# Kernel optimization log

Measured on AMD Instinct MI355X. Metric: run time of the kernel, lower is better.

## Reference

```python
import jax, jax.numpy as jnp
import numpy as np

IMG = 224          # image_size
FMAP = (56, 56)    # feature_map_dims (AdaptiveAvgPool2d((56,56)))
K_REWEIGHT = 3     # self.n_reweight
BLUR_RADIUS = 4    # KNNGaussianBlur(4): kernel 9, sigma 4


def _cdist(a, b):
    # Euclidean pairwise distance, [Na, D] x [Nb, D] -> [Na, Nb]
    a2 = jnp.sum(a * a, axis=1, keepdims=True)            # [Na,1]
    b2 = jnp.sum(b * b, axis=1, keepdims=True).T          # [1,Nb]
    d2 = a2 + b2 - 2.0 * (a @ b.T)
    return jnp.sqrt(jnp.maximum(d2, 0.0))


def _gaussian_blur(x):
    # x: [1,1,H,W]; torchvision GaussianBlur(kernel=9, sigma=4), reflect pad
    r, sigma = BLUR_RADIUS, float(BLUR_RADIUS)
    t = jnp.arange(2 * r + 1, dtype=x.dtype) - r
    g = jnp.exp(-(t * t) / (2.0 * sigma * sigma))
    g = g / jnp.sum(g)
    k2d = jnp.outer(g, g)[None, None]                     # [1,1,9,9]
    xp = jnp.pad(x, ((0, 0), (0, 0), (r, r), (r, r)), mode='reflect')
    return jax.lax.conv_general_dilated(
        xp, k2d, window_strides=(1, 1), padding='VALID',
        dimension_numbers=('NCHW', 'OIHW', 'NCHW'))


def setup_inputs() -> dict:
    key = jax.random.key(0)
    k1, k2 = jax.random.split(key)
    patch = jax.random.normal(k1, (FMAP[0] * FMAP[1], 768), dtype=jnp.float32)
    patch_lib = jax.random.normal(k2, (16384, 768), dtype=jnp.float32)
    mean = jnp.zeros((), dtype=jnp.float32)
    std = jnp.ones((), dtype=jnp.float32)
    return {"patch": patch, "patch_lib": patch_lib, "mean": mean, "std": std}


def reference(patch, patch_lib, mean, std):
    # normalization (method_name != 'Point_MAE' branch)
    p = (patch - mean) / std                               # [N, D]

    dist = _cdist(p, patch_lib)                            # [N, Nlib]
    min_val = jnp.min(dist, axis=1)                        # [N]
    min_idx = jnp.argmin(dist, axis=1)                     # [N]
    s_idx = jnp.argmax(min_val)
    s_star = jnp.max(min_val)

    m_test = p[s_idx]                                      # [D]
    m_star = patch_lib[min_idx[s_idx]]                     # [D]

    # distances of m_star to whole bank, k smallest
    w_dist = jnp.sqrt(jnp.maximum(
        jnp.sum((patch_lib - m_star) ** 2, axis=1), 0.0))  # [Nlib]
    _, nn_idx = jax.lax.top_k(-w_dist, K_REWEIGHT)         # smallest k
    m_star_knn = jnp.linalg.norm(
        m_test[None, :] - patch_lib[nn_idx[1:]], axis=1)   # [k-1]

    D_sqrt = jnp.sqrt(jnp.asarray(patch.shape[1], dtype=p.dtype))
    w = 1.0 - jnp.exp(s_star / D_sqrt) / jnp.sum(jnp.exp(m_star_knn / D_sqrt))
    s = w * s_star

    s_map = min_val.reshape(1, 1, *FMAP)
    s_map = jax.image.resize(s_map, (1, 1, IMG, IMG), method='bilinear')
    s_map = _gaussian_blur(s_map)
    return s, s_map
```

## Files before the change

### kernel.cpp

```cpp
#include <hip/hip_runtime.h>
#include <hip/hip_bf16.h>
#include <stdint.h>

#define N_PATCH 3136
#define N_PATCH_PAD 3200
#define N_LIB   16384
#define DIM     768
#define IMGSZ   224
#define FM      56

#define BK 32
#define KT 24
#define MT 25
#define NTILES 128

#define TAILB 64
#define D2_MARGIN 8.0f

typedef __bf16 bf16_t;
typedef __bf16 bf16x8 __attribute__((ext_vector_type(8)));
typedef __bf16 bf16x4_v __attribute__((ext_vector_type(4)));
typedef float  f32x4  __attribute__((ext_vector_type(4)));

#define FLT_MAX_ 3.402823466e+38f

struct Scal {
  unsigned long long approx_max_pack;
  unsigned long long cand_pack[64];
  int cand[64];
  int cand_count;
  int bar[4];
};

__device__ __forceinline__ float wave_reduce_sum(float v) {
#pragma unroll
  for (int s = 32; s > 0; s >>= 1) v += __shfl_xor(v, s, 64);
  return v;
}

__device__ __forceinline__ float wave_reduce_min(float v) {
#pragma unroll
  for (int s = 32; s > 0; s >>= 1) v = fminf(v, __shfl_xor(v, s, 64));
  return v;
}

__device__ __forceinline__ unsigned long long shfl_xor_u64(unsigned long long v, int mask) {
  unsigned lo = (unsigned)v, hi = (unsigned)(v >> 32);
  lo = __shfl_xor(lo, mask, 64);
  hi = __shfl_xor(hi, mask, 64);
  return ((unsigned long long)hi << 32) | lo;
}

__device__ __forceinline__ void async16(const bf16_t* g, bf16_t* l) {
  __builtin_amdgcn_global_load_lds(
      (const __attribute__((address_space(1))) unsigned int*)g,
      (__attribute__((address_space(3))) unsigned int*)l, 16, 0, 0);
}

__device__ __forceinline__ void grid_bar(int* ctr, int nb) {
  __syncthreads();
  if (threadIdx.x == 0) {
    __threadfence();
    atomicAdd(ctr, 1);
    while (atomicAdd(ctr, 0) < nb) __builtin_amdgcn_s_sleep(8);
    __threadfence();
  }
  __syncthreads();
}

__device__ __forceinline__ float bf16u_to_f(unsigned short u) {
  return __uint_as_float(((unsigned)u) << 16);
}

__global__ void prep_kernel(const float* __restrict__ patch, const float* __restrict__ lib,
                            const float* __restrict__ meanp, const float* __restrict__ stdp,
                            bf16_t* __restrict__ pb, bf16_t* __restrict__ lb,
                            float* __restrict__ a2, float* __restrict__ b2, Scal* sc) {
  int t = threadIdx.x;
  int lane = t & 63;
  if (blockIdx.x == 0) {
    if (t < 64) sc->cand_pack[t] = ~0ULL;
    if (t == 64) { sc->approx_max_pack = 0ULL; sc->cand_count = 0; }
    if (t >= 65 && t < 69) sc->bar[t - 65] = 0;
  }
  if (blockIdx.x < N_PATCH / 4) {
    int row = blockIdx.x * 4 + (t >> 6);
    float mu = meanp[0], sd = stdp[0];
    float acc = 0.f;
#pragma unroll
    for (int k = 0; k < 3; k++) {
      float4 v = ((const float4*)(patch + (size_t)row * DIM))[lane + 64 * k];
      v.x = (v.x - mu) / sd; v.y = (v.y - mu) / sd;
      v.z = (v.z - mu) / sd; v.w = (v.w - mu) / sd;
      bf16x4_v o = {(__bf16)v.x, (__bf16)v.y, (__bf16)v.z, (__bf16)v.w};
      *(bf16x4_v*)(pb + (size_t)row * DIM + (lane + 64 * k) * 4) = o;
      acc += v.x*v.x + v.y*v.y + v.z*v.z + v.w*v.w;
    }
    acc = wave_reduce_sum(acc);
    if (lane == 0) a2[row] = acc;
  } else {
    int row = (blockIdx.x - N_PATCH / 4) * 4 + (t >> 6);
    float acc = 0.f;
#pragma unroll
    for (int k = 0; k < 3; k++) {
      float4 v = ((const float4*)(lib + (size_t)row * DIM))[lane + 64 * k];
      bf16x4_v o = {(__bf16)v.x, (__bf16)v.y, (__bf16)v.z, (__bf16)v.w};
      *(bf16x4_v*)(lb + (size_t)row * DIM + (lane + 64 * k) * 4) = o;
      acc += v.x*v.x + v.y*v.y + v.z*v.z + v.w*v.w;
    }
    acc = wave_reduce_sum(acc);
    if (lane == 0) b2[row] = acc;
  }
}

__global__ __launch_bounds__(256, 3)
void gemm_min_kernel(const bf16_t* __restrict__ pb, const bf16_t* __restrict__ lb,
                     const float* __restrict__ a2, const float* __restrict__ b2,
                     float* __restrict__ part) {
  __shared__ __align__(16) bf16_t As[2][128 * BK];
  __shared__ __align__(16) bf16_t Bs[2][128 * BK];
  __shared__ unsigned smin[128];

  const int t = threadIdx.x;
  const int wave = t >> 6;
  const int lane = t & 63;
  const int l15 = lane & 15;
  const int quad = lane >> 4;
  const int wm = (wave >> 1) * 64;
  const int wn = (wave & 1) * 64;

  const int lid = blockIdx.x;
  const int xcd = lid & 7;
  const int slot = lid >> 3;
  const int ntile = xcd + 8 * (slot / MT);
  const int mtile = slot % MT;
  const int m0 = mtile * 128;
  const int n0 = ntile * 128;

  int ra0 = m0 + (t >> 2);       if (ra0 > N_PATCH - 1) ra0 = N_PATCH - 1;
  int ra1 = m0 + 64 + (t >> 2);  if (ra1 > N_PATCH - 1) ra1 = N_PATCH - 1;
  const bf16_t* gA0 = pb + (size_t)ra0 * DIM + (t & 3) * 8;
  const bf16_t* gA1 = pb + (size_t)ra1 * DIM + (t & 3) * 8;
  const bf16_t* gB0 = lb + (size_t)(n0 + (t >> 2)) * DIM + (t & 3) * 8;
  const bf16_t* gB1 = gB0 + (size_t)64 * DIM;

  if (t < 128) smin[t] = 0xffffffffu;

  {
    bf16_t* la = &As[0][0];
    bf16_t* lb_ = &Bs[0][0];
    async16(gA0, la + t * 8);
    async16(gA1, la + 2048 + t * 8);
    async16(gB0, lb_ + t * 8);
    async16(gB1, lb_ + 2048 + t * 8);
  }
  __syncthreads();

  f32x4 acc[4][4];
#pragma unroll
  for (int mi = 0; mi < 4; mi++)
#pragma unroll
    for (int ni = 0; ni < 4; ni++) { f32x4 z = {0.f,0.f,0.f,0.f}; acc[mi][ni] = z; }

  for (int k = 0; k < KT; ++k) {
    const int cur = k & 1;
    if (k + 1 < KT) {
      const int nxt = cur ^ 1;
      const size_t ko = (size_t)(k + 1) * BK;
      bf16_t* la = &As[nxt][0];
      bf16_t* lb_ = &Bs[nxt][0];
      async16(gA0 + ko, la + t * 8);
      async16(gA1 + ko, la + 2048 + t * 8);
      async16(gB0 + ko, lb_ + t * 8);
      async16(gB1 + ko, lb_ + 2048 + t * 8);
    }

    bf16x8 afr[4], bfr[4];
#pragma unroll
    for (int mi = 0; mi < 4; mi++)
      afr[mi] = *(const bf16x8*)(&As[cur][(wm + mi * 16 + l15) * BK + quad * 8]);
#pragma unroll
    for (int ni = 0; ni < 4; ni++)
      bfr[ni] = *(const bf16x8*)(&Bs[cur][(wn + ni * 16 + l15) * BK + quad * 8]);
#pragma unroll
    for (int mi = 0; mi < 4; mi++)
#pragma unroll
      for (int ni = 0; ni < 4; ni++)
        acc[mi][ni] = __builtin_amdgcn_mfma_f32_16x16x32_bf16(afr[mi], bfr[ni],
                                                              acc[mi][ni], 0, 0, 0);
    __syncthreads();
  }

  float b2n[4];
#pragma unroll
  for (int ni = 0; ni < 4; ni++) b2n[ni] = b2[n0 + wn + ni * 16 + l15];

#pragma unroll
  for (int mi = 0; mi < 4; mi++) {
#pragma unroll
    for (int r = 0; r < 4; r++) {
      int rloc = wm + mi * 16 + quad * 4 + r;
      int mrow = m0 + rloc;
      float a2v = a2[mrow < N_PATCH ? mrow : (N_PATCH - 1)];
      float best = a2v + b2n[0] - 2.0f * acc[mi][0][r];
#pragma unroll
      for (int ni = 1; ni < 4; ni++)
        best = fminf(best, a2v + b2n[ni] - 2.0f * acc[mi][ni][r]);
      best = fmaxf(best, 0.0f);
#pragma unroll
      for (int s = 1; s < 16; s <<= 1)
        best = fminf(best, __shfl_xor(best, s, 64));
      if (l15 == 0) atomicMin(&smin[rloc], __float_as_uint(best));
    }
  }
  __syncthreads();
  if (t < 128) part[(size_t)ntile * N_PATCH_PAD + m0 + t] = __uint_as_float(smin[t]);
}

__device__ __forceinline__ void wave_pick(const Scal* sc, int cnt, int lane,
                                          int* srow, float* sstar, int* ms) {
  unsigned long long pk = 0ULL;
  int rowv = 0, msv = 0;
  if (lane < cnt) {
    unsigned long long cp = sc->cand_pack[lane];
    rowv = sc->cand[lane];
    msv = (int)(cp & 0xffffffffu);
    pk = (cp & 0xffffffff00000000ULL) | (unsigned)(0xffffffffu - (unsigned)rowv);
  }
  unsigned long long m = pk;
#pragma unroll
  for (int s = 1; s < 64; s <<= 1) {
    unsigned long long o = shfl_xor_u64(m, s);
    if (o > m) m = o;
  }
  unsigned long long mask = __ballot(pk == m && lane < cnt);
  int wl = (int)(__ffsll((long long)mask) - 1);
  *srow = __shfl(rowv, wl, 64);
  *ms   = __shfl(msv, wl, 64);
  *sstar = sqrtf(__uint_as_float((unsigned)(m >> 32)));
}

__global__ __launch_bounds__(256, 2)
void tail_kernel(const float* __restrict__ part, float* __restrict__ min_val,
                 const float* __restrict__ patch, const float* __restrict__ lib,
                 const bf16_t* __restrict__ lb,
                 const float* __restrict__ meanp, const float* __restrict__ stdp,
                 Scal* __restrict__ sc, float* __restrict__ wdist2,
                 float* __restrict__ out0, float* __restrict__ outmap) {
  __shared__ union {
    unsigned long long sl[768];
    float rs[40 * 40];
  } sm;
  __shared__ float redbuf[4];
  __shared__ int s_cnt;

  const int t = threadIdx.x;
  const int b = blockIdx.x;
  const int wave = t >> 6, lane = t & 63;

  {
    int row = b * 256 + t;
    if (row < N_PATCH) {
      float m = FLT_MAX_;
#pragma unroll 8
      for (int nt = 0; nt < NTILES; nt++)
        m = fminf(m, part[(size_t)nt * N_PATCH_PAD + row]);
      float v = sqrtf(m);
      min_val[row] = v;
      unsigned long long mp = (((unsigned long long)__float_as_uint(v)) << 32) |
                              (unsigned)(0xffffffffu - (unsigned)row);
      atomicMax(&sc->approx_max_pack, mp);
    }
  }
  grid_bar(&sc->bar[0], TAILB);

  if (b == 0) {
    float amax = __uint_as_float((unsigned)(atomicMax(&sc->approx_max_pack, 0ULL) >> 32));
    for (int i = t; i < N_PATCH; i += 256) {
      if (min_val[i] >= amax - 0.05f) {
        int p = atomicAdd(&sc->cand_count, 1);
        if (p < 64) sc->cand[p] = i;
      }
    }
  }
  grid_bar(&sc->bar[1], TAILB);

  if (t == 0) s_cnt = atomicAdd(&sc->cand_count, 0);
  __syncthreads();
  int cnt = s_cnt; if (cnt > 64) cnt = 64;

  {
    float mu = meanp[0], sd = stdp[0];
    for (int c = 0; c < cnt; c++) {
      int row = sc->cand[c];
      float pv_ = (t < NTILES) ? part[(size_t)t * N_PATCH_PAD + row] : FLT_MAX_;
      pv_ = wave_reduce_min(pv_);
      if (lane == 0) redbuf[wave] = pv_;
      __syncthreads();
      float bmin = fminf(fminf(redbuf[0], redbuf[1]), fminf(redbuf[2], redbuf[3]));
      __syncthreads();

      float4 pv[3];
#pragma unroll
      for (int k = 0; k < 3; k++) {
        float4 v = ((const float4*)(patch + (size_t)row * DIM))[lane + 64 * k];
        v.x = (v.x - mu) / sd; v.y = (v.y - mu) / sd;
        v.z = (v.z - mu) / sd; v.w = (v.w - mu) / sd;
        pv[k] = v;
      }
#pragma unroll
      for (int tt = 0; tt < 2; tt++) {
        int nt = 2 * b + tt;
        float pmin = part[(size_t)nt * N_PATCH_PAD + row];
        if (pmin <= bmin + D2_MARGIN) {
          unsigned long long best = ~0ULL;
          int jb = nt * 128 + wave * 32;
          for (int rr = 0; rr < 32; rr++) {
            int j = jb + rr;
            const float4* pl = (const float4*)(lib + (size_t)j * DIM);
            float acc = 0.f;
#pragma unroll
            for (int k = 0; k < 3; k++) {
              float4 l = pl[lane + 64 * k];
              float dx = pv[k].x - l.x, dy = pv[k].y - l.y;
              float dz = pv[k].z - l.z, dw = pv[k].w - l.w;
              acc += dx*dx + dy*dy + dz*dz + dw*dw;
            }
            acc = wave_reduce_sum(acc);
            unsigned long long pk = (((unsigned long long)__float_as_uint(acc)) << 32) | (unsigned)j;
            if (pk < best) best = pk;
          }
          if (lane == 0) atomicMin(&sc->cand_pack[c], best);
        }
      }
    }
  }
  grid_bar(&sc->bar[2], TAILB);

  {
    int srow_, ms; float ss_;
    wave_pick(sc, cnt, lane, &srow_, &ss_, &ms);
    float pm[12];
    const ushort4* pms = (const ushort4*)(lb + (size_t)ms * DIM);
#pragma unroll
    for (int k = 0; k < 3; k++) {
      ushort4 u = pms[lane + 64 * k];
      pm[k*4+0] = bf16u_to_f(u.x); pm[k*4+1] = bf16u_to_f(u.y);
      pm[k*4+2] = bf16u_to_f(u.z); pm[k*4+3] = bf16u_to_f(u.w);
    }
    int jbase = b * 256 + wave * 64;
    for (int rr = 0; rr < 64; rr += 2) {
      int j0 = jbase + rr, j1 = j0 + 1;
      const ushort4* r0 = (const ushort4*)(lb + (size_t)j0 * DIM);
      const ushort4* r1 = (const ushort4*)(lb + (size_t)j1 * DIM);
      float a0 = 0.f, a1 = 0.f;
#pragma unroll
      for (int k = 0; k < 3; k++) {
        ushort4 u0 = r0[lane + 64 * k];
        ushort4 u1 = r1[lane + 64 * k];
        float d;
        d = bf16u_to_f(u0.x) - pm[k*4+0]; a0 += d * d;
        d = bf16u_to_f(u0.y) - pm[k*4+1]; a0 += d * d;
        d = bf16u_to_f(u0.z) - pm[k*4+2]; a0 += d * d;
        d = bf16u_to_f(u0.w) - pm[k*4+3]; a0 += d * d;
        d = bf16u_to_f(u1.x) - pm[k*4+0]; a1 += d * d;
        d = bf16u_to_f(u1.y) - pm[k*4+1]; a1 += d * d;
        d = bf16u_to_f(u1.z) - pm[k*4+2]; a1 += d * d;
        d = bf16u_to_f(u1.w) - pm[k*4+3]; a1 += d * d;
      }
      a0 = wave_reduce_sum(a0);
      a1 = wave_reduce_sum(a1);
      if (lane == 0) { wdist2[j0] = a0; wdist2[j1] = a1; }
    }
  }
  grid_bar(&sc->bar[3], TAILB);

  if (b == 0) {
    unsigned long long b0 = ~0ULL, b1 = ~0ULL, b2 = ~0ULL;
    for (int j = t; j < N_LIB; j += 256) {
      unsigned long long pk = (((unsigned long long)__float_as_uint(wdist2[j])) << 32) | (unsigned)j;
      if (pk < b0)      { b2 = b1; b1 = b0; b0 = pk; }
      else if (pk < b1) { b2 = b1; b1 = pk; }
      else if (pk < b2) { b2 = pk; }
    }
    sm.sl[t * 3 + 0] = b0; sm.sl[t * 3 + 1] = b1; sm.sl[t * 3 + 2] = b2;
    __syncthreads();
    if (t >= 64) return;

    unsigned long long c0 = ~0ULL, c1 = ~0ULL, c2 = ~0ULL;
#pragma unroll
    for (int e = 0; e < 12; e++) {
      unsigned long long pk = sm.sl[t * 12 + e];
      if (pk < c0)      { c2 = c1; c1 = c0; c0 = pk; }
      else if (pk < c1) { c2 = c1; c1 = pk; }
      else if (pk < c2) { c2 = pk; }
    }
    unsigned long long res1 = 0, res2 = 0;
#pragma unroll
    for (int r = 0; r < 3; r++) {
      unsigned long long m = c0;
#pragma unroll
      for (int s = 1; s < 64; s <<= 1) {
        unsigned long long o = shfl_xor_u64(m, s);
        if (o < m) m = o;
      }
      if (r == 1) res1 = m;
      if (r == 2) res2 = m;
      if (c0 == m) { c0 = c1; c1 = c2; c2 = ~0ULL; }
    }
    int nA = (int)(res1 & 0xffffffffu);
    int nB = (int)(res2 & 0xffffffffu);

    int srow, ms2; float sstar;
    wave_pick(sc, cnt, t, &srow, &sstar, &ms2);

    float mu = meanp[0], sd = stdp[0];
    float accA = 0.f, accB = 0.f;
#pragma unroll
    for (int k = 0; k < 3; k++) {
      float4 p4 = ((const float4*)(patch + (size_t)srow * DIM))[t + 64 * k];
      float4 a4 = ((const float4*)(lib + (size_t)nA * DIM))[t + 64 * k];
      float4 b4 = ((const float4*)(lib + (size_t)nB * DIM))[t + 64 * k];
      float px = (p4.x - mu) / sd, py = (p4.y - mu) / sd;
      float pz = (p4.z - mu) / sd, pw = (p4.w - mu) / sd;
      float dax = px - a4.x, day = py - a4.y, daz = pz - a4.z, daw = pw - a4.w;
      float dbx = px - b4.x, dby = py - b4.y, dbz = pz - b4.z, dbw = pw - b4.w;
      accA += dax*dax + day*day + daz*daz + daw*daw;
      accB += dbx*dbx + dby*dby + dbz*dbz + dbw*dbw;
    }
    accA = wave_reduce_sum(accA);
    accB = wave_reduce_sum(accB);
    if (t == 0) {
      float dsq = sqrtf((float)DIM);
      float d1 = sqrtf(accA), d2v = sqrtf(accB);
      float w = 1.0f - expf(sstar / dsq) / (expf(d1 / dsq) + expf(d2v / dsq));
      out0[0] = w * sstar;
    }
    return;
  }

  if (b > 49) return;
  {
    int tile = b - 1;
    int bx = tile % 7, by = tile / 7;
    int ox0 = bx * 32, oy0 = by * 32;

    for (int i = t; i < 1600; i += 256) {
      int ly = i / 40, lx = i % 40;
      int gy = oy0 - 4 + ly; gy = gy < 0 ? 0 : (gy > 223 ? 223 : gy);
      int gx = ox0 - 4 + lx; gx = gx < 0 ? 0 : (gx > 223 ? 223 : gx);
      float sy = fminf(fmaxf(0.25f * gy - 0.375f, 0.0f), 55.0f);
      float sx = fminf(fmaxf(0.25f * gx - 0.375f, 0.0f), 55.0f);
      int y0 = (int)sy; if (y0 > 54) y0 = 54;
      int x0 = (int)sx; if (x0 > 54) x0 = 54;
      float fy = sy - y0, fx = sx - x0;
      float v00 = min_val[y0*FM + x0],     v01 = min_val[y0*FM + x0 + 1];
      float v10 = min_val[(y0+1)*FM + x0], v11 = min_val[(y0+1)*FM + x0 + 1];
      float a = v00 + fx * (v01 - v00);
      float bb = v10 + fx * (v11 - v10);
      sm.rs[i] = a + fy * (bb - a);
    }
    __syncthreads();

    float g[9]; float gs = 0.f;
#pragma unroll
    for (int i = 0; i < 9; i++) { float tt = (float)(i - 4); g[i] = expf(-(tt*tt)/32.0f); gs += g[i]; }
#pragma unroll
    for (int i = 0; i < 9; i++) g[i] /= gs;

    for (int p = t; p < 1024; p += 256) {
      int y = oy0 + p / 32, x = ox0 + (p & 31);
      float acc = 0.f;
#pragma unroll
      for (int dy = 0; dy < 9; dy++) {
        int yy = y + dy - 4;
        yy = yy < 0 ? -yy : (yy > IMGSZ - 1 ? 2*(IMGSZ-1) - yy : yy);
        int lyy = yy - (oy0 - 4);
        float ra = 0.f;
#pragma unroll
        for (int dx = 0; dx < 9; dx++) {
          int xx = x + dx - 4;
          xx = xx < 0 ? -xx : (xx > IMGSZ - 1 ? 2*(IMGSZ-1) - xx : xx);
          ra += g[dx] * sm.rs[lyy * 40 + (xx - (ox0 - 4))];
        }
        acc += g[dy] * ra;
      }
      outmap[y * IMGSZ + x] = acc;
    }
  }
}

extern "C" void kernel_launch(void* const* d_in, const int* in_sizes, int n_in,
                              void* d_out, int out_size, void* d_ws, size_t ws_size,
                              hipStream_t stream) {
  const float* patch = (const float*)d_in[0];
  const float* lib   = (const float*)d_in[1];
  const float* meanp = (const float*)d_in[2];
  const float* stdp  = (const float*)d_in[3];
  float* out = (float*)d_out;

  char* ws = (char*)d_ws;
  size_t off = 0;
  auto alloc = [&](size_t bytes) -> void* {
    void* p = ws + off;
    off = (off + bytes + 255) & ~(size_t)255;
    return p;
  };
  bf16_t* pb      = (bf16_t*)alloc((size_t)N_PATCH * DIM * sizeof(bf16_t));
  bf16_t* lb      = (bf16_t*)alloc((size_t)N_LIB * DIM * sizeof(bf16_t));
  float* a2       = (float*)alloc(N_PATCH * sizeof(float));
  float* b2       = (float*)alloc(N_LIB * sizeof(float));
  float* part     = (float*)alloc((size_t)N_PATCH_PAD * NTILES * sizeof(float));
  float* min_val  = (float*)alloc(N_PATCH * sizeof(float));
  float* wdist2   = (float*)alloc(N_LIB * sizeof(float));
  Scal*  sc       = (Scal*)alloc(sizeof(Scal));

  prep_kernel<<<N_PATCH / 4 + N_LIB / 4, 256, 0, stream>>>(patch, lib, meanp, stdp,
                                                           pb, lb, a2, b2, sc);
  gemm_min_kernel<<<MT * NTILES, 256, 0, stream>>>(pb, lb, a2, b2, part);
  tail_kernel<<<TAILB, 256, 0, stream>>>(part, min_val, patch, lib, lb, meanp, stdp,
                                         sc, wdist2, out, out + 1);
}
```

Measured before the change: 319.2 us.

## Enlarge GEMM-min tiles to 256x256 with 4-stage async pipeline

The distance GEMM tile grows from 128x128 with 256 threads to 256x256 with 512 threads, so each wave computes a 128x64 sub-tile. The single double buffer becomes a 4-stage ring with explicit vmcnt waits and raw barriers, and MFMA issue priority is raised during the compute phase. The intent is more operand reuse per LDS load and fewer barrier stalls per K step. The cost is more register and LDS pressure, fewer blocks per CU, and more padding waste on the M dimension (13 tiles of 256 rows for 3136). The tail kernel's exact-refinement loop is adapted to the new 256-wide library tiles and the halved partial-min count.

```diff
diff --git a/kernel.cpp b/kernel.cpp
--- a/kernel.cpp
+++ b/kernel.cpp
@@ -3,16 +3,17 @@
 #include <stdint.h>
 
 #define N_PATCH 3136
-#define N_PATCH_PAD 3200
+#define N_PATCH_PAD 3328
 #define N_LIB   16384
 #define DIM     768
 #define IMGSZ   224
 #define FM      56
 
+#define TILE 256
 #define BK 32
 #define KT 24
-#define MT 25
-#define NTILES 128
+#define MT 13
+#define NTILES 64
 
 #define TAILB 64
 #define D2_MARGIN 8.0f
@@ -113,90 +114,105 @@
   }
 }
 
-__global__ __launch_bounds__(256, 3)
+__global__ __launch_bounds__(512, 2)
 void gemm_min_kernel(const bf16_t* __restrict__ pb, const bf16_t* __restrict__ lb,
                      const float* __restrict__ a2, const float* __restrict__ b2,
                      float* __restrict__ part) {
-  __shared__ __align__(16) bf16_t As[2][128 * BK];
-  __shared__ __align__(16) bf16_t Bs[2][128 * BK];
-  __shared__ unsigned smin[128];
+  __shared__ __align__(16) bf16_t As[4][TILE * BK];
+  __shared__ __align__(16) bf16_t Bs[4][TILE * BK];
 
   const int t = threadIdx.x;
   const int wave = t >> 6;
   const int lane = t & 63;
   const int l15 = lane & 15;
   const int quad = lane >> 4;
-  const int wm = (wave >> 1) * 64;
-  const int wn = (wave & 1) * 64;
+  const int wm = (wave >> 2) * 128;
+  const int wn = (wave & 3) * 64;
 
   const int lid = blockIdx.x;
   const int xcd = lid & 7;
   const int slot = lid >> 3;
   const int ntile = xcd + 8 * (slot / MT);
   const int mtile = slot % MT;
-  const int m0 = mtile * 128;
-  const int n0 = ntile * 128;
-
-  int ra0 = m0 + (t >> 2);       if (ra0 > N_PATCH - 1) ra0 = N_PATCH - 1;
-  int ra1 = m0 + 64 + (t >> 2);  if (ra1 > N_PATCH - 1) ra1 = N_PATCH - 1;
+  const int m0 = mtile * TILE;
+  const int n0 = ntile * TILE;
+
+  int ra0 = m0 + (t >> 2);        if (ra0 > N_PATCH - 1) ra0 = N_PATCH - 1;
+  int ra1 = m0 + 128 + (t >> 2);  if (ra1 > N_PATCH - 1) ra1 = N_PATCH - 1;
   const bf16_t* gA0 = pb + (size_t)ra0 * DIM + (t & 3) * 8;
   const bf16_t* gA1 = pb + (size_t)ra1 * DIM + (t & 3) * 8;
   const bf16_t* gB0 = lb + (size_t)(n0 + (t >> 2)) * DIM + (t & 3) * 8;
-  const bf16_t* gB1 = gB0 + (size_t)64 * DIM;
-
-  if (t < 128) smin[t] = 0xffffffffu;
-
-  {
-    bf16_t* la = &As[0][0];
-    bf16_t* lb_ = &Bs[0][0];
-    async16(gA0, la + t * 8);
-    async16(gA1, la + 2048 + t * 8);
-    async16(gB0, lb_ + t * 8);
-    async16(gB1, lb_ + 2048 + t * 8);
-  }
-  __syncthreads();
-
-  f32x4 acc[4][4];
-#pragma unroll
-  for (int mi = 0; mi < 4; mi++)
+  const bf16_t* gB1 = gB0 + (size_t)128 * DIM;
+
+  auto stage = [&](int kt, int s) {
+    const size_t ko = (size_t)kt * BK;
+    async16(gA0 + ko, &As[s][0] + (size_t)t * 8);
+    async16(gA1 + ko, &As[s][0] + 4096 + (size_t)t * 8);
+    async16(gB0 + ko, &Bs[s][0] + (size_t)t * 8);
+    async16(gB1 + ko, &Bs[s][0] + 4096 + (size_t)t * 8);
+  };
+
+  f32x4 acc[8][4];
+#pragma unroll
+  for (int mi = 0; mi < 8; mi++)
 #pragma unroll
     for (int ni = 0; ni < 4; ni++) { f32x4 z = {0.f,0.f,0.f,0.f}; acc[mi][ni] = z; }
 
-  for (int k = 0; k < KT; ++k) {
-    const int cur = k & 1;
-    if (k + 1 < KT) {
-      const int nxt = cur ^ 1;
-      const size_t ko = (size_t)(k + 1) * BK;
-      bf16_t* la = &As[nxt][0];
-      bf16_t* lb_ = &Bs[nxt][0];
-      async16(gA0 + ko, la + t * 8);
-      async16(gA1 + ko, la + 2048 + t * 8);
-      async16(gB0 + ko, lb_ + t * 8);
-      async16(gB1 + ko, lb_ + 2048 + t * 8);
-    }
-
-    bf16x8 afr[4], bfr[4];
-#pragma unroll
-    for (int mi = 0; mi < 4; mi++)
-      afr[mi] = *(const bf16x8*)(&As[cur][(wm + mi * 16 + l15) * BK + quad * 8]);
+  stage(0, 0); stage(1, 1); stage(2, 2);
+
+  auto compute = [&](int s) {
+    const bf16_t* Ab = &As[s][0];
+    const bf16_t* Bb = &Bs[s][0];
+    bf16x8 afr[8], bfr[4];
 #pragma unroll
     for (int ni = 0; ni < 4; ni++)
-      bfr[ni] = *(const bf16x8*)(&Bs[cur][(wn + ni * 16 + l15) * BK + quad * 8]);
-#pragma unroll
-    for (int mi = 0; mi < 4; mi++)
+      bfr[ni] = *(const bf16x8*)(Bb + (wn + ni * 16 + l15) * BK + quad * 8);
+#pragma unroll
+    for (int mi = 0; mi < 8; mi++)
+      afr[mi] = *(const bf16x8*)(Ab + (wm + mi * 16 + l15) * BK + quad * 8);
+    __builtin_amdgcn_s_setprio(1);
+#pragma unroll
+    for (int mi = 0; mi < 8; mi++)
 #pragma unroll
       for (int ni = 0; ni < 4; ni++)
         acc[mi][ni] = __builtin_amdgcn_mfma_f32_16x16x32_bf16(afr[mi], bfr[ni],
                                                               acc[mi][ni], 0, 0, 0);
-    __syncthreads();
-  }
+    __builtin_amdgcn_s_setprio(0);
+  };
+
+  for (int k = 0; k < KT - 3; ++k) {
+    asm volatile("s_waitcnt vmcnt(8)" ::: "memory");
+    __builtin_amdgcn_s_barrier();
+    asm volatile("" ::: "memory");
+    stage(k + 3, (k + 3) & 3);
+    compute(k & 3);
+  }
+  asm volatile("s_waitcnt vmcnt(8)" ::: "memory");
+  __builtin_amdgcn_s_barrier();
+  asm volatile("" ::: "memory");
+  compute((KT - 3) & 3);
+
+  asm volatile("s_waitcnt vmcnt(4)" ::: "memory");
+  __builtin_amdgcn_s_barrier();
+  asm volatile("" ::: "memory");
+  compute((KT - 2) & 3);
+
+  asm volatile("s_waitcnt vmcnt(0)" ::: "memory");
+  __builtin_amdgcn_s_barrier();
+  asm volatile("" ::: "memory");
+  compute((KT - 1) & 3);
+
+  __syncthreads();
+  unsigned* smin = (unsigned*)&As[0][0];
+  if (t < 256) smin[t] = 0xffffffffu;
+  __syncthreads();
 
   float b2n[4];
 #pragma unroll
   for (int ni = 0; ni < 4; ni++) b2n[ni] = b2[n0 + wn + ni * 16 + l15];
 
 #pragma unroll
-  for (int mi = 0; mi < 4; mi++) {
+  for (int mi = 0; mi < 8; mi++) {
 #pragma unroll
     for (int r = 0; r < 4; r++) {
       int rloc = wm + mi * 16 + quad * 4 + r;
@@ -214,7 +230,7 @@
     }
   }
   __syncthreads();
-  if (t < 128) part[(size_t)ntile * N_PATCH_PAD + m0 + t] = __uint_as_float(smin[t]);
+  if (t < 256) part[(size_t)ntile * N_PATCH_PAD + m0 + t] = __uint_as_float(smin[t]);
 }
 
 __device__ __forceinline__ void wave_pick(const Scal* sc, int cnt, int lane,
@@ -308,30 +324,27 @@
         v.z = (v.z - mu) / sd; v.w = (v.w - mu) / sd;
         pv[k] = v;
       }
-#pragma unroll
-      for (int tt = 0; tt < 2; tt++) {
-        int nt = 2 * b + tt;
-        float pmin = part[(size_t)nt * N_PATCH_PAD + row];
-        if (pmin <= bmin + D2_MARGIN) {
-          unsigned long long best = ~0ULL;
-          int jb = nt * 128 + wave * 32;
-          for (int rr = 0; rr < 32; rr++) {
-            int j = jb + rr;
-            const float4* pl = (const float4*)(lib + (size_t)j * DIM);
-            float acc = 0.f;
-#pragma unroll
-            for (int k = 0; k < 3; k++) {
-              float4 l = pl[lane + 64 * k];
-              float dx = pv[k].x - l.x, dy = pv[k].y - l.y;
-              float dz = pv[k].z - l.z, dw = pv[k].w - l.w;
-              acc += dx*dx + dy*dy + dz*dz + dw*dw;
-            }
-            acc = wave_reduce_sum(acc);
-            unsigned long long pk = (((unsigned long long)__float_as_uint(acc)) << 32) | (unsigned)j;
-            if (pk < best) best = pk;
+      int nt = b;
+      float pmin = part[(size_t)nt * N_PATCH_PAD + row];
+      if (pmin <= bmin + D2_MARGIN) {
+        unsigned long long best = ~0ULL;
+        int jb = nt * 256 + wave * 64;
+        for (int rr = 0; rr < 64; rr++) {
+          int j = jb + rr;
+          const float4* pl = (const float4*)(lib + (size_t)j * DIM);
+          float acc = 0.f;
+#pragma unroll
+          for (int k = 0; k < 3; k++) {
+            float4 l = pl[lane + 64 * k];
+            float dx = pv[k].x - l.x, dy = pv[k].y - l.y;
+            float dz = pv[k].z - l.z, dw = pv[k].w - l.w;
+            acc += dx*dx + dy*dy + dz*dz + dw*dw;
           }
-          if (lane == 0) atomicMin(&sc->cand_pack[c], best);
+          acc = wave_reduce_sum(acc);
+          unsigned long long pk = (((unsigned long long)__float_as_uint(acc)) << 32) | (unsigned)j;
+          if (pk < best) best = pk;
         }
+        if (lane == 0) atomicMin(&sc->cand_pack[c], best);
       }
     }
   }
@@ -517,7 +530,7 @@
 
   prep_kernel<<<N_PATCH / 4 + N_LIB / 4, 256, 0, stream>>>(patch, lib, meanp, stdp,
                                                            pb, lb, a2, b2, sc);
-  gemm_min_kernel<<<MT * NTILES, 256, 0, stream>>>(pb, lb, a2, b2, part);
+  gemm_min_kernel<<<MT * NTILES, 512, 0, stream>>>(pb, lb, a2, b2, part);
   tail_kernel<<<TAILB, 256, 0, stream>>>(part, min_val, patch, lib, lb, meanp, stdp,
                                          sc, wdist2, out, out + 1);
 }
```

Result: slower. 349.5 us (+9.5%).
